# Performance work log

Hardware: AMD Instinct MI355X
Metric: run time of the kernel (lower is better)

## Reference

```python
import jax, jax.numpy as jnp
import numpy as np

DIM = 512
HEADS = 8
DH = DIM // HEADS          # 64, dim_head = dim // 8
M = DIM // 2               # 256 landmarks
ITERS = 6                  # pinv iterations
KS = 33                    # residual depthwise conv kernel (lucidrains default)
N_LAYERS = 2
LN_EPS = 1e-5


def layer_norm(x, scale, bias):
    mu = x.mean(-1, keepdims=True)
    var = ((x - mu) ** 2).mean(-1, keepdims=True)
    return (x - mu) * jax.lax.rsqrt(var + LN_EPS) * scale + bias


def sinusoidal_pe(T, d, dtype):
    pos = np.arange(T)[:, None]
    div = np.exp(np.arange(0, d, 2) * (-np.log(10000.0) / d))
    pe = np.zeros((T, d), dtype=np.float32)
    pe[:, 0::2] = np.sin(pos * div)
    pe[:, 1::2] = np.cos(pos * div)
    return jnp.asarray(pe, dtype=dtype)


def iter_pinv(x):
    # Newton-Schulz Moore-Penrose iteration (lucidrains), global-max scaling
    ax = jnp.abs(x)
    denom = ax.sum(-1).max() * ax.sum(-2).max()
    z = jnp.swapaxes(x, -1, -2) / denom
    I = jnp.eye(x.shape[-1], dtype=x.dtype)
    for _ in range(ITERS):
        xz = x @ z
        z = 0.25 * (z @ (13.0 * I - xz @ (15.0 * I - xz @ (7.0 * I - xz))))
    return z


def nystrom_attention(x, qkv_w, out_w, out_b, conv_w):
    b, n, d = x.shape
    pad = (-n) % M                       # left-pad so seq divisible by M
    xp = jnp.pad(x, ((0, 0), (pad, 0), (0, 0)))
    N = n + pad
    q, k, v = [t.reshape(b, N, HEADS, DH).transpose(0, 2, 1, 3)
               for t in jnp.split(xp @ qkv_w, 3, axis=-1)]  # each [b,h,N,dh]
    q = q * (DH ** -0.5)
    l = N // M                           # segment length per landmark
    q_l = q.reshape(b, HEADS, M, l, DH).mean(3)   # [b,h,M,dh]
    k_l = k.reshape(b, HEADS, M, l, DH).mean(3)
    attn1 = jax.nn.softmax(jnp.einsum('bhid,bhjd->bhij', q, k_l), -1)    # [b,h,N,M]
    attn2 = jax.nn.softmax(jnp.einsum('bhid,bhjd->bhij', q_l, k_l), -1)  # [b,h,M,M]
    attn3 = jax.nn.softmax(jnp.einsum('bhid,bhjd->bhij', q_l, k), -1)    # [b,h,M,N]
    out = attn1 @ (iter_pinv(attn2) @ (attn3 @ v))                       # [b,h,N,dh]
    # residual depthwise conv over sequence, per head (groups=heads)
    P = KS // 2
    out = out + jax.lax.conv_general_dilated(
        v, conv_w, (1, 1), ((P, P), (0, 0)),
        dimension_numbers=('NCHW', 'OIHW', 'NCHW'), feature_group_count=HEADS)
    out = out.transpose(0, 2, 1, 3).reshape(b, N, d)
    out = out @ out_w + out_b
    return out[:, -n:]


def setup_inputs() -> dict:
    key = jax.random.key(0)
    ks = jax.random.split(key, 12)
    B, T, IN_DIM = 4, 4095, 1024
    s = 0.02
    return {
        'data': jax.random.normal(ks[0], (B, T, IN_DIM), jnp.float32),
        'fc1_w': jax.random.normal(ks[1], (IN_DIM, DIM), jnp.float32) * s,
        'fc1_b': jnp.zeros((DIM,), jnp.float32),
        'cls_token': jax.random.normal(ks[2], (1, 1, DIM), jnp.float32),
        'ln_scale': jnp.ones((N_LAYERS, DIM), jnp.float32),
        'ln_bias': jnp.zeros((N_LAYERS, DIM), jnp.float32),
        'qkv_w': jax.random.normal(ks[3], (N_LAYERS, DIM, 3 * DIM), jnp.float32) * s,
        'out_w': jax.random.normal(ks[4], (N_LAYERS, DIM, DIM), jnp.float32) * s,
        'out_b': jnp.zeros((N_LAYERS, DIM), jnp.float32),
        'conv_w': jax.random.normal(ks[5], (N_LAYERS, HEADS, 1, KS, 1), jnp.float32) * s,
        'fnorm_scale': jnp.ones((DIM,), jnp.float32),
        'fnorm_bias': jnp.zeros((DIM,), jnp.float32),
        'fcout_w': jax.random.normal(ks[6], (DIM, 1), jnp.float32) * s,
        'fcout_b': jnp.zeros((1,), jnp.float32),
    }


def reference(data, fc1_w, fc1_b, cls_token, ln_scale, ln_bias, qkv_w, out_w,
              out_b, conv_w, fnorm_scale, fnorm_bias, fcout_w, fcout_b):
    B, T, _ = data.shape
    h = jax.nn.relu(data @ fc1_w + fc1_b)
    h = h + sinusoidal_pe(T, DIM, h.dtype)
    cls = jnp.broadcast_to(cls_token, (B, 1, DIM))
    h = jnp.concatenate([cls, h], axis=1)
    for i in range(N_LAYERS):
        h = h + nystrom_attention(layer_norm(h, ln_scale[i], ln_bias[i]),
                                  qkv_w[i], out_w[i], out_b[i], conv_w[i])
    h = layer_norm(h, fnorm_scale, fnorm_bias)
    logits = (h[:, 0] @ fcout_w + fcout_b)[:, 0]
    y_prob = jax.nn.sigmoid(logits)
    y_hat = (y_prob > 0.5).astype(jnp.int32)
    return logits, y_prob, y_hat
```

## Files before the change

kernel.cpp:

```cpp
#include <hip/hip_runtime.h>
#include <math.h>

typedef long long ll;
typedef __attribute__((ext_vector_type(8))) short short8;
typedef __attribute__((ext_vector_type(4))) float f32x4;

#define NBATCH 4
#define TSEQ   4095
#define NTOK   4096
#define DMODEL 512
#define NHEAD  8
#define DHEAD  64
#define NLAND  256
#define INDIM  1024
#define KCONV  33
#define NBH    32
#define NSPLIT 8

__device__ __forceinline__ float bred(float* red, float v, int tid, int op){
  red[tid] = v; __syncthreads();
  for (int s = 128; s > 0; s >>= 1){
    if (tid < s) red[tid] = op ? fmaxf(red[tid], red[tid+s]) : (red[tid] + red[tid+s]);
    __syncthreads();
  }
  float r = red[0];
  __syncthreads();
  return r;
}

__device__ __forceinline__ short f2bf(float f){
  unsigned u = __float_as_uint(f);
  u += 0x7fff + ((u>>16)&1);
  return (short)(u>>16);
}
__device__ __forceinline__ float bf2f(short s){
  return __uint_as_float(((unsigned)(unsigned short)s) << 16);
}

__device__ __forceinline__ void gload16(const void* g, void* l){
  __builtin_amdgcn_global_load_lds((const __attribute__((address_space(1))) void*)g,
                                   (__attribute__((address_space(3))) void*)l, 16, 0, 0);
}

__global__ __launch_bounds__(256) void pe_table_k(float* __restrict__ pe){
  int idx = blockIdx.x*256 + threadIdx.x;
  if (idx >= TSEQ*DMODEL) return;
  int c = idx & 511; int t = idx >> 9;
  const double NEG = -9.210340371976184 / 512.0;
  double div = exp((double)(c & ~1) * NEG);
  float ang = (float)((double)t * div);
  pe[idx] = (c & 1) ? cosf(ang) : sinf(ang);
}

__global__ __launch_bounds__(256) void pe_cls_add_k(float* __restrict__ hb, const float* __restrict__ cls,
                                                    const float* __restrict__ pe){
  ll idx = (ll)blockIdx.x*256 + threadIdx.x;
  int c = (int)(idx & 511);
  ll rn = idx >> 9;
  int n = (int)(rn & 4095);
  if (n == 0) hb[idx] = cls[c];
  else        hb[idx] += pe[(ll)(n-1)*512 + c];
}

__global__ __launch_bounds__(256) void cvt_bf16_k(const float* __restrict__ in, short* __restrict__ out, int n8){
  int idx = blockIdx.x*256 + threadIdx.x;
  for (int i = idx; i < n8; i += gridDim.x*256){
    const f32x4* p = (const f32x4*)(in + (ll)i*8);
    f32x4 a = p[0], b = p[1];
    short8 v;
    v[0]=f2bf(a[0]); v[1]=f2bf(a[1]); v[2]=f2bf(a[2]); v[3]=f2bf(a[3]);
    v[4]=f2bf(b[0]); v[5]=f2bf(b[1]); v[6]=f2bf(b[2]); v[7]=f2bf(b[3]);
    ((short8*)out)[i] = v;
  }
}

__global__ __launch_bounds__(256) void transpose_bf16_k(const float* __restrict__ in, short* __restrict__ out,
                                                        int K, int N, ll sIn, ll sOut){
  __shared__ float t[64][65];
  int L = blockIdx.z;
  in  += (ll)L*sIn;
  out += (ll)L*sOut;
  int n0 = blockIdx.x*64, k0 = blockIdx.y*64;
  int tid = threadIdx.x;
  for (int e = tid; e < 4096; e += 256){
    int r = e >> 6, c = e & 63;
    t[r][c] = in[(ll)(k0 + r)*N + n0 + c];
  }
  __syncthreads();
  for (int e = tid; e < 4096; e += 256){
    int r = e >> 6, c = e & 63;
    out[(ll)(n0 + r)*K + k0 + c] = f2bf(t[c][r]);
  }
}

__global__ __launch_bounds__(256) void ln_rows_k(const float* __restrict__ in, short* __restrict__ out,
                                                 const float* __restrict__ sc, const float* __restrict__ bi){
  __shared__ float red[256];
  ll row = blockIdx.x;
  const float* xr = in + row*DMODEL;
  short* orow = out + row*DMODEL;
  int tid = threadIdx.x;
  float v0 = xr[tid], v1 = xr[tid+256];
  float mu = bred(red, v0+v1, tid, 0) * (1.f/512.f);
  float d0 = v0-mu, d1 = v1-mu;
  float var = bred(red, d0*d0 + d1*d1, tid, 0) * (1.f/512.f);
  float inv = 1.f / sqrtf(var + 1e-5f);
  orow[tid]     = f2bf(d0*inv*sc[tid]     + bi[tid]);
  orow[tid+256] = f2bf(d1*inv*sc[tid+256] + bi[tid+256]);
}

template<int BM, int BN, int AB, int BMODE, int CB, int SW>
__global__ __launch_bounds__(256)
void mgemm(const void* __restrict__ Av, const void* __restrict__ Bv,
           void* __restrict__ Cv, const void* __restrict__ Ev,
           const float* __restrict__ bias,
           int Mr, int K, int lda, int ldb, int ldc,
           ll sA, ll sB, ll sC,
           float c0, float c1, int flags)
{
  constexpr int MI = BM/32, NJ = BN/32;
  __shared__ __align__(16) short As[BM*64];
  __shared__ __align__(16) short Bs[BN*64];
  int z = blockIdx.z;
  int bx = blockIdx.x, by = blockIdx.y;
  if (SW){
    int nwg = gridDim.x*gridDim.y;
    int lin = by*gridDim.x + bx;
    int q = nwg >> 3, r = nwg & 7;
    int xcd = lin & 7, idx = lin >> 3;
    int wg = (xcd < r) ? (xcd*(q+1) + idx) : (r*(q+1) + (xcd - r)*q + idx);
    bx = wg % gridDim.x; by = wg / gridDim.x;
  }
  int n0 = bx*BN, m0 = by*BM;
  int tid = threadIdx.x;
  int lane = tid & 63, w = tid >> 6;
  int wr = w >> 1, wc = w & 1;
  int l15 = lane & 15, l4 = lane >> 4;
  bool fullM = (m0 + BM <= Mr);

  f32x4 acc[MI][NJ];
  #pragma unroll
  for (int i = 0; i < MI; i++)
    #pragma unroll
    for (int j = 0; j < NJ; j++) acc[i][j] = (f32x4){0.f,0.f,0.f,0.f};

  for (int k0 = 0; k0 < K; k0 += 64){
    if (AB && fullM){
      #pragma unroll
      for (int it = 0; it < BM/32; ++it){
        int base = (w*(BM/32) + it)*64;
        int ls = base + lane;
        int row = ls >> 3, slot = ls & 7;
        const short* gp = (const short*)Av + (ll)z*sA + (ll)(m0 + row)*lda + k0 + ((slot ^ (row&7))<<3);
        gload16(gp, (char*)As + (ll)base*16);
      }
    } else {
      #pragma unroll
      for (int it = 0; it < BM/32; ++it){
        int tau = tid + 256*it;
        int row = tau >> 3, slot = tau & 7;
        int grow = m0 + row;
        short8 v;
        if (AB){
          if (grow < Mr) v = *(const short8*)((const short*)Av + (ll)z*sA + (ll)grow*lda + k0 + slot*8);
          else v = (short8){0,0,0,0,0,0,0,0};
        } else {
          f32x4 p0 = {0.f,0.f,0.f,0.f}, p1 = {0.f,0.f,0.f,0.f};
          if (grow < Mr){
            const float* ap = (const float*)Av + (ll)z*sA + (ll)grow*lda + k0 + slot*8;
            p0 = *(const f32x4*)ap; p1 = *(const f32x4*)(ap+4);
          }
          v[0]=f2bf(p0[0]); v[1]=f2bf(p0[1]); v[2]=f2bf(p0[2]); v[3]=f2bf(p0[3]);
          v[4]=f2bf(p1[0]); v[5]=f2bf(p1[1]); v[6]=f2bf(p1[2]); v[7]=f2bf(p1[3]);
        }
        ((short8*)As)[row*8 + (slot ^ (row&7))] = v;
      }
    }
    if (BMODE == 2){
      #pragma unroll
      for (int it = 0; it < BN/32; ++it){
        int base = (w*(BN/32) + it)*64;
        int ls = base + lane;
        int n = ls >> 3, slot = ls & 7;
        const short* gp = (const short*)Bv + (ll)z*sB + (ll)(n0 + n)*ldb + k0 + ((slot ^ (n&7))<<3);
        gload16(gp, (char*)Bs + (ll)base*16);
      }
    } else {
      #pragma unroll
      for (int it = 0; it < BN/32; ++it){
        int tau = tid + 256*it;
        int n = tau & (BN-1), slot = tau >> (BN==128 ? 7 : 6);
        short8 v;
        if (BMODE == 1){
          const short* bp = (const short*)Bv + (ll)z*sB + (ll)(k0 + slot*8)*ldb + n0 + n;
          #pragma unroll
          for (int i = 0; i < 8; i++) v[i] = bp[(ll)i*ldb];
        } else {
          const float* bp = (const float*)Bv + (ll)z*sB + (ll)(k0 + slot*8)*ldb + n0 + n;
          #pragma unroll
          for (int i = 0; i < 8; i++) v[i] = f2bf(bp[(ll)i*ldb]);
        }
        ((short8*)Bs)[n*8 + (slot ^ (n&7))] = v;
      }
    }
    __syncthreads();
    #pragma unroll
    for (int kc = 0; kc < 2; kc++){
      short8 af[MI], bfr[NJ];
      #pragma unroll
      for (int i = 0; i < MI; i++){
        int row = wr*(BM/2) + i*16 + l15;
        int g = kc*4 + l4;
        af[i] = ((short8*)As)[row*8 + (g ^ (row&7))];
      }
      #pragma unroll
      for (int j = 0; j < NJ; j++){
        int col = wc*(BN/2) + j*16 + l15;
        int g = kc*4 + l4;
        bfr[j] = ((short8*)Bs)[col*8 + (g ^ (col&7))];
      }
      #pragma unroll
      for (int i = 0; i < MI; i++)
        #pragma unroll
        for (int j = 0; j < NJ; j++)
          acc[i][j] = __builtin_amdgcn_mfma_f32_16x16x32_bf16(af[i], bfr[j], acc[i][j], 0, 0, 0);
    }
    __syncthreads();
  }

  #pragma unroll
  for (int i = 0; i < MI; i++){
    int rbase = m0 + wr*(BM/2) + i*16 + l4*4;
    #pragma unroll
    for (int j = 0; j < NJ; j++){
      int col = n0 + wc*(BN/2) + j*16 + l15;
      #pragma unroll
      for (int r = 0; r < 4; r++){
        int m = rbase + r;
        if (m >= Mr) continue;
        float v = acc[i][j][r];
        if (flags & 4){
          float ev = CB ? bf2f(((const short*)Ev + (ll)z*sC)[(ll)m*ldc + col])
                        : ((const float*)Ev + (ll)z*sC)[(ll)m*ldc + col];
          v = c0 * ev + c1 * v;
        }
        if (flags & 1) v += bias[col];
        if (flags & 2) v = fmaxf(v, 0.f);
        int om = (flags & 16) ? (m + m/TSEQ + 1) : m;
        ll ci = (ll)z*sC + (ll)om*ldc + col;
        if (CB){
          short* Cs = (short*)Cv;
          if (flags & 8) v += bf2f(Cs[ci]);
          Cs[ci] = f2bf(v);
        } else {
          float* Cf = (float*)Cv;
          if (flags & 8) v += Cf[ci];
          Cf[ci] = v;
        }
      }
    }
  }
}

__global__ __launch_bounds__(256)
void gemm_nt(const short* __restrict__ A, const short* __restrict__ Bm, float* __restrict__ C,
             int lda, int ldb, int ldc,
             ll sAb, ll sAh, ll sBb, ll sBh, ll sCb, ll sCh,
             float alpha)
{
  __shared__ float As[64][65];
  __shared__ float Bs[64][65];
  int z = blockIdx.z; int b = z >> 3; int h = z & 7;
  A  += (ll)b*sAb + (ll)h*sAh;
  Bm += (ll)b*sBb + (ll)h*sBh;
  C  += (ll)b*sCb + (ll)h*sCh;
  int n0 = blockIdx.x*64, m0 = blockIdx.y*64;
  int tid = threadIdx.x;
  int kk = tid & 63, rr = tid >> 6;
  #pragma unroll
  for (int r = 0; r < 16; r++){
    As[rr + 4*r][kk] = bf2f(A [(ll)(m0 + rr + 4*r)*lda + kk]);
    Bs[rr + 4*r][kk] = bf2f(Bm[(ll)(n0 + rr + 4*r)*ldb + kk]);
  }
  __syncthreads();
  int tx = tid & 15, ty = tid >> 4;
  float acc[4][4] = {};
  for (int k = 0; k < 64; k++){
    float a[4], bv[4];
    #pragma unroll
    for (int i = 0; i < 4; i++) a[i] = As[ty + 16*i][k];
    #pragma unroll
    for (int j = 0; j < 4; j++) bv[j] = Bs[tx + 16*j][k];
    #pragma unroll
    for (int i = 0; i < 4; i++)
      #pragma unroll
      for (int j = 0; j < 4; j++)
        acc[i][j] += a[i]*bv[j];
  }
  #pragma unroll
  for (int i = 0; i < 4; i++)
    #pragma unroll
    for (int j = 0; j < 4; j++)
      C[(ll)(m0 + ty + 16*i)*ldc + n0 + tx + 16*j] = alpha * acc[i][j];
}

__global__ __launch_bounds__(256)
void mflash_k(const short* __restrict__ Q, const short* __restrict__ K,
              const short* __restrict__ V, short* __restrict__ O,
              int ldq, int ldk, int ldv, int ldo, int nkeys, float alpha,
              ll sQb, ll sQh, ll sKb, ll sKh, ll sVb, ll sVh, ll sOb, ll sOh)
{
  __shared__ __align__(16) short Qs[64*64];
  __shared__ __align__(16) short Ks[64*64];
  __shared__ __align__(16) short Vs[64*64];
  __shared__ __align__(16) short Ps[64*64];
  __shared__ float Sl[64][68];
  __shared__ float m_l[64], s_l[64], scl[64];
  int z = blockIdx.z; int b = z >> 3; int h = z & 7;
  Q += (ll)b*sQb + (ll)h*sQh;
  K += (ll)b*sKb + (ll)h*sKh;
  V += (ll)b*sVb + (ll)h*sVh;
  O += (ll)b*sOb + (ll)h*sOh;
  int m0 = blockIdx.x*64;
  int tid = threadIdx.x;
  int lane = tid & 63, w = tid >> 6;
  int l15 = lane & 15, l4 = lane >> 4;
  int wr = w >> 1, wc = w & 1;

  #pragma unroll
  for (int it = 0; it < 2; it++){
    int tau = tid + 256*it;
    int row = tau >> 3, slot = tau & 7;
    short8 v = *(const short8*)(Q + (ll)(m0 + row)*ldq + slot*8);
    ((short8*)Qs)[row*8 + (slot ^ (row&7))] = v;
  }
  if (tid < 64){ m_l[tid] = -1e30f; s_l[tid] = 0.f; }
  f32x4 o[2][2];
  #pragma unroll
  for (int i = 0; i < 2; i++)
    #pragma unroll
    for (int j = 0; j < 2; j++) o[i][j] = (f32x4){0.f,0.f,0.f,0.f};

  for (int n0 = 0; n0 < nkeys; n0 += 64){
    __syncthreads();
    #pragma unroll
    for (int it = 0; it < 2; it++){
      int tau = tid + 256*it;
      int row = tau >> 3, slot = tau & 7;
      short8 v = *(const short8*)(K + (ll)(n0 + row)*ldk + slot*8);
      ((short8*)Ks)[row*8 + (slot ^ (row&7))] = v;
    }
    #pragma unroll
    for (int it = 0; it < 2; it++){
      int key = (tid >> 3) + 32*it;
      int d0 = (tid & 7)*8;
      short8 v = *(const short8*)(V + (ll)(n0 + key)*ldv + d0);
      #pragma unroll
      for (int j = 0; j < 8; j++){
        int d = d0 + j;
        Vs[d*64 + (((key>>3) ^ (d&7))<<3) + (key&7)] = v[j];
      }
    }
    __syncthreads();
    f32x4 s[2][2];
    #pragma unroll
    for (int i = 0; i < 2; i++)
      #pragma unroll
      for (int j = 0; j < 2; j++) s[i][j] = (f32x4){0.f,0.f,0.f,0.f};
    #pragma unroll
    for (int kc = 0; kc < 2; kc++){
      short8 aq[2], bk[2];
      int g = kc*4 + l4;
      #pragma unroll
      for (int i = 0; i < 2; i++){
        int row = wr*32 + i*16 + l15;
        aq[i] = ((short8*)Qs)[row*8 + (g ^ (row&7))];
      }
      #pragma unroll
      for (int j = 0; j < 2; j++){
        int key = wc*32 + j*16 + l15;
        bk[j] = ((short8*)Ks)[key*8 + (g ^ (key&7))];
      }
      #pragma unroll
      for (int i = 0; i < 2; i++)
        #pragma unroll
        for (int j = 0; j < 2; j++)
          s[i][j] = __builtin_amdgcn_mfma_f32_16x16x32_bf16(aq[i], bk[j], s[i][j], 0, 0, 0);
    }
    #pragma unroll
    for (int i = 0; i < 2; i++)
      #pragma unroll
      for (int j = 0; j < 2; j++)
        #pragma unroll
        for (int r = 0; r < 4; r++)
          Sl[wr*32 + i*16 + l4*4 + r][wc*32 + j*16 + l15] = s[i][j][r] * alpha;
    __syncthreads();
    {
      int row = tid >> 2, q = tid & 3, cb = q*16;
      float sv[16];
      float cmax = -1e30f;
      #pragma unroll
      for (int cc = 0; cc < 16; cc++){ sv[cc] = Sl[row][cb+cc]; cmax = fmaxf(cmax, sv[cc]); }
      cmax = fmaxf(cmax, __shfl_xor(cmax, 1));
      cmax = fmaxf(cmax, __shfl_xor(cmax, 2));
      float mprev = m_l[row];
      float newm = fmaxf(mprev, cmax);
      float lsum = 0.f;
      short8 pv0, pv1;
      #pragma unroll
      for (int cc = 0; cc < 8; cc++){ float e = expf(sv[cc]-newm); lsum += e; pv0[cc] = f2bf(e); }
      #pragma unroll
      for (int cc = 0; cc < 8; cc++){ float e = expf(sv[8+cc]-newm); lsum += e; pv1[cc] = f2bf(e); }
      lsum += __shfl_xor(lsum, 1);
      lsum += __shfl_xor(lsum, 2);
      ((short8*)Ps)[row*8 + ((2*q)   ^ (row&7))] = pv0;
      ((short8*)Ps)[row*8 + ((2*q+1) ^ (row&7))] = pv1;
      if (q == 0){
        float scale = expf(mprev - newm);
        m_l[row] = newm;
        s_l[row] = s_l[row]*scale + lsum;
        scl[row] = scale;
      }
    }
    __syncthreads();
    #pragma unroll
    for (int i = 0; i < 2; i++)
      #pragma unroll
      for (int r = 0; r < 4; r++){
        float sc = scl[wr*32 + i*16 + l4*4 + r];
        #pragma unroll
        for (int j = 0; j < 2; j++) o[i][j][r] *= sc;
      }
    #pragma unroll
    for (int kc = 0; kc < 2; kc++){
      short8 ap[2], bv[2];
      int g = kc*4 + l4;
      #pragma unroll
      for (int i = 0; i < 2; i++){
        int row = wr*32 + i*16 + l15;
        ap[i] = ((short8*)Ps)[row*8 + (g ^ (row&7))];
      }
      #pragma unroll
      for (int j = 0; j < 2; j++){
        int d = wc*32 + j*16 + l15;
        bv[j] = ((short8*)Vs)[d*8 + (g ^ (d&7))];
      }
      #pragma unroll
      for (int i = 0; i < 2; i++)
        #pragma unroll
        for (int j = 0; j < 2; j++)
          o[i][j] = __builtin_amdgcn_mfma_f32_16x16x32_bf16(ap[i], bv[j], o[i][j], 0, 0, 0);
    }
  }
  #pragma unroll
  for (int i = 0; i < 2; i++)
    #pragma unroll
    for (int j = 0; j < 2; j++)
      #pragma unroll
      for (int r = 0; r < 4; r++){
        int row = wr*32 + i*16 + l4*4 + r;
        int col = wc*32 + j*16 + l15;
        O[(ll)(m0 + row)*ldo + col] = f2bf(o[i][j][r] / s_l[row]);
      }
}

__global__ __launch_bounds__(256)
void mflash3_part_k(const short* __restrict__ Q, const short* __restrict__ K,
                    const short* __restrict__ V,
                    float* __restrict__ po, float* __restrict__ pm, float* __restrict__ pl,
                    int ldq, int ldk, int ldv,
                    ll sQb, ll sQh, ll sKb, ll sKh, ll sVb, ll sVh)
{
  __shared__ __align__(16) short Qs[64*64];
  __shared__ __align__(16) short Ks[64*64];
  __shared__ __align__(16) short Vs[64*64];
  __shared__ __align__(16) short Ps[64*64];
  __shared__ float Sl[64][68];
  __shared__ float m_l[64], s_l[64], scl[64];
  int z = blockIdx.z; int b = z >> 3; int h = z & 7;
  int split = blockIdx.y;
  Q += (ll)b*sQb + (ll)h*sQh;
  K += (ll)b*sKb + (ll)h*sKh;
  V += (ll)b*sVb + (ll)h*sVh;
  int m0 = blockIdx.x*64;
  int koff = split * (NTOK/NSPLIT);
  int tid = threadIdx.x;
  int lane = tid & 63, w = tid >> 6;
  int l15 = lane & 15, l4 = lane >> 4;
  int wr = w >> 1, wc = w & 1;

  #pragma unroll
  for (int it = 0; it < 2; it++){
    int tau = tid + 256*it;
    int row = tau >> 3, slot = tau & 7;
    short8 v = *(const short8*)(Q + (ll)(m0 + row)*ldq + slot*8);
    ((short8*)Qs)[row*8 + (slot ^ (row&7))] = v;
  }
  if (tid < 64){ m_l[tid] = -1e30f; s_l[tid] = 0.f; }
  f32x4 o[2][2];
  #pragma unroll
  for (int i = 0; i < 2; i++)
    #pragma unroll
    for (int j = 0; j < 2; j++) o[i][j] = (f32x4){0.f,0.f,0.f,0.f};

  for (int n0 = koff; n0 < koff + NTOK/NSPLIT; n0 += 64){
    __syncthreads();
    #pragma unroll
    for (int it = 0; it < 2; it++){
      int tau = tid + 256*it;
      int row = tau >> 3, slot = tau & 7;
      short8 v = *(const short8*)(K + (ll)(n0 + row)*ldk + slot*8);
      ((short8*)Ks)[row*8 + (slot ^ (row&7))] = v;
    }
    #pragma unroll
    for (int it = 0; it < 2; it++){
      int key = (tid >> 3) + 32*it;
      int d0 = (tid & 7)*8;
      short8 v = *(const short8*)(V + (ll)(n0 + key)*ldv + d0);
      #pragma unroll
      for (int j = 0; j < 8; j++){
        int d = d0 + j;
        Vs[d*64 + (((key>>3) ^ (d&7))<<3) + (key&7)] = v[j];
      }
    }
    __syncthreads();
    f32x4 s[2][2];
    #pragma unroll
    for (int i = 0; i < 2; i++)
      #pragma unroll
      for (int j = 0; j < 2; j++) s[i][j] = (f32x4){0.f,0.f,0.f,0.f};
    #pragma unroll
    for (int kc = 0; kc < 2; kc++){
      short8 aq[2], bk[2];
      int g = kc*4 + l4;
      #pragma unroll
      for (int i = 0; i < 2; i++){
        int row = wr*32 + i*16 + l15;
        aq[i] = ((short8*)Qs)[row*8 + (g ^ (row&7))];
      }
      #pragma unroll
      for (int j = 0; j < 2; j++){
        int key = wc*32 + j*16 + l15;
        bk[j] = ((short8*)Ks)[key*8 + (g ^ (key&7))];
      }
      #pragma unroll
      for (int i = 0; i < 2; i++)
        #pragma unroll
        for (int j = 0; j < 2; j++)
          s[i][j] = __builtin_amdgcn_mfma_f32_16x16x32_bf16(aq[i], bk[j], s[i][j], 0, 0, 0);
    }
    #pragma unroll
    for (int i = 0; i < 2; i++)
      #pragma unroll
      for (int j = 0; j < 2; j++)
        #pragma unroll
        for (int r = 0; r < 4; r++)
          Sl[wr*32 + i*16 + l4*4 + r][wc*32 + j*16 + l15] = s[i][j][r];
    __syncthreads();
    {
      int row = tid >> 2, q = tid & 3, cb = q*16;
      float sv[16];
      float cmax = -1e30f;
      #pragma unroll
      for (int cc = 0; cc < 16; cc++){ sv[cc] = Sl[row][cb+cc]; cmax = fmaxf(cmax, sv[cc]); }
      cmax = fmaxf(cmax, __shfl_xor(cmax, 1));
      cmax = fmaxf(cmax, __shfl_xor(cmax, 2));
      float mprev = m_l[row];
      float newm = fmaxf(mprev, cmax);
      float lsum = 0.f;
      short8 pv0, pv1;
      #pragma unroll
      for (int cc = 0; cc < 8; cc++){ float e = expf(sv[cc]-newm); lsum += e; pv0[cc] = f2bf(e); }
      #pragma unroll
      for (int cc = 0; cc < 8; cc++){ float e = expf(sv[8+cc]-newm); lsum += e; pv1[cc] = f2bf(e); }
      lsum += __shfl_xor(lsum, 1);
      lsum += __shfl_xor(lsum, 2);
      ((short8*)Ps)[row*8 + ((2*q)   ^ (row&7))] = pv0;
      ((short8*)Ps)[row*8 + ((2*q+1) ^ (row&7))] = pv1;
      if (q == 0){
        float scale = expf(mprev - newm);
        m_l[row] = newm;
        s_l[row] = s_l[row]*scale + lsum;
        scl[row] = scale;
      }
    }
    __syncthreads();
    #pragma unroll
    for (int i = 0; i < 2; i++)
      #pragma unroll
      for (int r = 0; r < 4; r++){
        float sc = scl[wr*32 + i*16 + l4*4 + r];
        #pragma unroll
        for (int j = 0; j < 2; j++) o[i][j][r] *= sc;
      }
    #pragma unroll
    for (int kc = 0; kc < 2; kc++){
      short8 ap[2], bv[2];
      int g = kc*4 + l4;
      #pragma unroll
      for (int i = 0; i < 2; i++){
        int row = wr*32 + i*16 + l15;
        ap[i] = ((short8*)Ps)[row*8 + (g ^ (row&7))];
      }
      #pragma unroll
      for (int j = 0; j < 2; j++){
        int d = wc*32 + j*16 + l15;
        bv[j] = ((short8*)Vs)[d*8 + (g ^ (d&7))];
      }
      #pragma unroll
      for (int i = 0; i < 2; i++)
        #pragma unroll
        for (int j = 0; j < 2; j++)
          o[i][j] = __builtin_amdgcn_mfma_f32_16x16x32_bf16(ap[i], bv[j], o[i][j], 0, 0, 0);
    }
  }
  int bs = z*NSPLIT + split;
  #pragma unroll
  for (int i = 0; i < 2; i++)
    #pragma unroll
    for (int j = 0; j < 2; j++)
      #pragma unroll
      for (int r = 0; r < 4; r++){
        int row = wr*32 + i*16 + l4*4 + r;
        int col = wc*32 + j*16 + l15;
        po[((ll)bs*NLAND + m0 + row)*64 + col] = o[i][j][r];
      }
  if (tid < 64){
    pm[(ll)bs*NLAND + m0 + tid] = m_l[tid];
    pl[(ll)bs*NLAND + m0 + tid] = s_l[tid];
  }
}

__global__ __launch_bounds__(256)
void flash3_comb_k(const float* __restrict__ po, const float* __restrict__ pm,
                   const float* __restrict__ pl, short* __restrict__ av){
  int bh = blockIdx.y;
  int row = blockIdx.x*4 + (threadIdx.x >> 6);
  int col = threadIdx.x & 63;
  float ms = -1e30f;
  float mv[NSPLIT];
  #pragma unroll
  for (int s = 0; s < NSPLIT; s++){
    mv[s] = pm[((ll)bh*NSPLIT + s)*NLAND + row];
    ms = fmaxf(ms, mv[s]);
  }
  float osum = 0.f, lsum = 0.f;
  #pragma unroll
  for (int s = 0; s < NSPLIT; s++){
    float wgt = expf(mv[s] - ms);
    osum += wgt * po[(((ll)bh*NSPLIT + s)*NLAND + row)*64 + col];
    lsum += wgt * pl[((ll)bh*NSPLIT + s)*NLAND + row];
  }
  av[((ll)bh*NLAND + row)*64 + col] = f2bf(osum / lsum);
}

__global__ __launch_bounds__(256) void softmax_rows_k(float* __restrict__ data, short* __restrict__ out16,
                                                      int cols){
  __shared__ float red[256];
  float* row = data + (ll)blockIdx.x * cols;
  short* row16 = out16 ? out16 + (ll)blockIdx.x * cols : nullptr;
  int tid = threadIdx.x;
  float m = -1e30f;
  for (int c = tid; c < cols; c += 256) m = fmaxf(m, row[c]);
  m = bred(red, m, tid, 1);
  float s = 0.f;
  for (int c = tid; c < cols; c += 256){ float e = expf(row[c] - m); row[c] = e; s += e; }
  s = bred(red, s, tid, 0);
  float inv = 1.f/s;
  for (int c = tid; c < cols; c += 256){
    float p = row[c] * inv;
    row[c] = p;
    if (row16) row16[c] = f2bf(p);
  }
}

__global__ __launch_bounds__(256) void landmarks_k(const short* __restrict__ qkv,
                                                   short* __restrict__ ql, short* __restrict__ kl){
  int idx = blockIdx.x*256 + threadIdx.x;
  int d = idx & 63;
  int i = (idx >> 6) & 255;
  int h = (idx >> 14) & 7;
  int b = idx >> 17;
  const short* base = qkv + ((ll)b*NTOK + (ll)i*16)*1536 + h*64 + d;
  float sq = 0.f, sk = 0.f;
  #pragma unroll
  for (int l = 0; l < 16; l++){ sq += bf2f(base[l*1536]); sk += bf2f(base[l*1536 + 512]); }
  ql[idx] = f2bf(sq * (0.125f/16.f));
  kl[idx] = f2bf(sk * (1.f/16.f));
}

__global__ void init_scal_k(unsigned* s){ s[0] = 0u; s[1] = 0u; }

__global__ __launch_bounds__(256) void a2_maxsums_k(const float* __restrict__ a2, unsigned* __restrict__ gm){
  __shared__ float red[256];
  const float* A = a2 + (ll)blockIdx.x*65536;
  int tid = threadIdx.x;
  float cs = 0.f, rs = 0.f;
  for (int i = 0; i < 256; i++) cs += A[i*256 + tid];
  for (int j = 0; j < 256; j++) rs += A[tid*256 + j];
  float cmax = bred(red, cs, tid, 1);
  float rmax = bred(red, rs, tid, 1);
  if (tid == 0){
    atomicMax(gm + 0, __float_as_uint(rmax));
    atomicMax(gm + 1, __float_as_uint(cmax));
  }
}

__global__ __launch_bounds__(256) void zinit_k(const float* __restrict__ a2, short* __restrict__ z,
                                               const unsigned* __restrict__ gm){
  float inv = 1.f / (__uint_as_float(gm[0]) * __uint_as_float(gm[1]));
  int idx = blockIdx.x*256 + threadIdx.x;
  int j = idx & 255, i = (idx >> 8) & 255, bh = idx >> 16;
  z[idx] = f2bf(a2[(ll)bh*65536 + j*256 + i] * inv);
}

__global__ __launch_bounds__(256) void dwconv_add_k(const short* __restrict__ qkv,
                                                    const float* __restrict__ cw, short* __restrict__ out){
  __shared__ float sv[160][64];
  int z = blockIdx.y; int b = z >> 3; int h = z & 7;
  int t0 = blockIdx.x * 128;
  int tid = threadIdx.x;
  const short* vbase = qkv + (ll)b*NTOK*1536 + 1024 + h*64;
  for (int e8 = tid; e8 < 1280; e8 += 256){
    int r = e8 >> 3, d8 = (e8 & 7)*8;
    int t = t0 - 16 + r;
    short8 v = (t >= 0 && t < NTOK) ? *(const short8*)(vbase + (ll)t*1536 + d8)
                                    : (short8){0,0,0,0,0,0,0,0};
    #pragma unroll
    for (int j = 0; j < 8; j++) sv[r][d8 + j] = bf2f(v[j]);
  }
  float wreg[KCONV];
  #pragma unroll
  for (int kk = 0; kk < KCONV; kk++) wreg[kk] = cw[h*KCONV + kk];
  __syncthreads();
  int d = tid & 63, g = tid >> 6;
  float vals[64];
  #pragma unroll
  for (int j = 0; j < 64; j++) vals[j] = sv[g*32 + j][d];
  short* obase = out + (ll)b*NTOK*512 + h*64 + d;
  #pragma unroll
  for (int t = 0; t < 32; t++){
    float s = 0.f;
    #pragma unroll
    for (int kk = 0; kk < KCONV; kk++) s += vals[t + kk]*wreg[kk];
    ll oi = (ll)(t0 + g*32 + t)*512;
    obase[oi] = f2bf(bf2f(obase[oi]) + s);
  }
}

__global__ __launch_bounds__(256) void head_k(const float* __restrict__ hb, const float* __restrict__ fns,
      const float* __restrict__ fnb, const float* __restrict__ fw, const float* __restrict__ fb,
      float* __restrict__ out){
  __shared__ float red[256];
  int b = blockIdx.x;
  const float* xr = hb + (ll)b*NTOK*DMODEL;
  int tid = threadIdx.x;
  float v0 = xr[tid], v1 = xr[tid+256];
  float mu = bred(red, v0+v1, tid, 0) * (1.f/512.f);
  float d0 = v0-mu, d1 = v1-mu;
  float var = bred(red, d0*d0 + d1*d1, tid, 0) * (1.f/512.f);
  float inv = 1.f/sqrtf(var + 1e-5f);
  float y0 = d0*inv*fns[tid]     + fnb[tid];
  float y1 = d1*inv*fns[tid+256] + fnb[tid+256];
  float dot = bred(red, y0*fw[tid] + y1*fw[tid+256], tid, 0);
  if (tid == 0){
    float logit = dot + fb[0];
    float prob = 1.f/(1.f + expf(-logit));
    out[b] = logit; out[4+b] = prob; out[8+b] = (prob > 0.5f) ? 1.f : 0.f;
  }
}

extern "C" void kernel_launch(void* const* d_in, const int* in_sizes, int n_in,
                              void* d_out, int out_size, void* d_ws, size_t ws_size,
                              hipStream_t stream)
{
  (void)in_sizes; (void)n_in; (void)out_size;
  const float* data  = (const float*)d_in[0];
  const float* fc1_w = (const float*)d_in[1];
  const float* fc1_b = (const float*)d_in[2];
  const float* cls   = (const float*)d_in[3];
  const float* ln_s  = (const float*)d_in[4];
  const float* ln_b  = (const float*)d_in[5];
  const float* qkv_w = (const float*)d_in[6];
  const float* out_w = (const float*)d_in[7];
  const float* out_b = (const float*)d_in[8];
  const float* convw = (const float*)d_in[9];
  const float* fns   = (const float*)d_in[10];
  const float* fnb   = (const float*)d_in[11];
  const float* fcw   = (const float*)d_in[12];
  const float* fcb   = (const float*)d_in[13];
  float* out = (float*)d_out;
  float* ws  = (float*)d_ws;

  float* h    = ws;
  short* xb   = (short*)(h + 8388608);
  short* qkvh = xb + 8388608;
  short* ql   = qkvh + 25165824;
  short* kl   = ql + 524288;
  float* a2f  = (float*)(kl + 524288);
  short* a2h  = (short*)(a2f + 2097152);
  short* zA   = a2h + 2097152;
  short* zB   = zA + 2097152;
  short* t1   = zB + 2097152;
  short* t2   = t1 + 2097152;
  short* t3   = t2 + 2097152;
  short* av   = t3 + 2097152;
  short* y2   = av + 524288;
  float* po   = (float*)(y2 + 524288);
  float* pm   = po + 4194304;
  float* pl   = pm + 65536;
  float* pe   = pl + 65536;
  short* datab = (short*)(pe + 2097152);
  short* fc1t  = datab + 16777216;
  short* qkvt  = fc1t + 524288;
  short* outt  = qkvt + 1572864;
  unsigned* scal = (unsigned*)(outt + 524288);

  const size_t NEED = (size_t)((char*)(scal + 2) - (char*)ws);
  if (ws_size < NEED) return;

  pe_table_k<<<(TSEQ*DMODEL + 255)/256, 256, 0, stream>>>(pe);
  cvt_bf16_k<<<2048, 256, 0, stream>>>(data, datab, (NBATCH*TSEQ*INDIM)/8);
  transpose_bf16_k<<<dim3(8, 16, 1), 256, 0, stream>>>(fc1_w, fc1t, INDIM, DMODEL, 0, 0);
  transpose_bf16_k<<<dim3(24, 8, 2), 256, 0, stream>>>(qkv_w, qkvt, DMODEL, 1536,
                                                       (ll)DMODEL*1536, (ll)1536*DMODEL);
  transpose_bf16_k<<<dim3(8, 8, 2), 256, 0, stream>>>(out_w, outt, DMODEL, DMODEL,
                                                      (ll)DMODEL*DMODEL, (ll)DMODEL*DMODEL);

  mgemm<128,128,1,2,0,1><<<dim3(4, 128, 1), 256, 0, stream>>>(
      datab, fc1t, h, nullptr, fc1_b,
      NBATCH*TSEQ, INDIM, INDIM, INDIM, DMODEL,
      0, 0, 0, 0.f, 0.f, 1|2|16);
  pe_cls_add_k<<<(NBATCH*NTOK*DMODEL)/256, 256, 0, stream>>>(h, cls, pe);

  for (int L = 0; L < 2; L++){
    const float* ob = out_b + (ll)L*DMODEL;
    const float* cw = convw + (ll)L*NHEAD*KCONV;
    const short* qwt = qkvt + (ll)L*1536*DMODEL;
    const short* owt = outt + (ll)L*DMODEL*DMODEL;

    ln_rows_k<<<NBATCH*NTOK, 256, 0, stream>>>(h, xb, ln_s + L*DMODEL, ln_b + L*DMODEL);
    mgemm<128,128,1,2,1,1><<<dim3(12, 128, 1), 256, 0, stream>>>(
        xb, qwt, qkvh, nullptr, nullptr,
        NBATCH*NTOK, DMODEL, DMODEL, DMODEL, 1536,
        0, 0, 0, 0.f, 0.f, 0);
    landmarks_k<<<2048, 256, 0, stream>>>(qkvh, ql, kl);

    gemm_nt<<<dim3(4, 4, NBH), 256, 0, stream>>>(
        ql, kl, a2f, 64, 64, 256,
        131072, 16384, 131072, 16384, 524288, 65536, 1.f);
    softmax_rows_k<<<NBH*NLAND, 256, 0, stream>>>(a2f, a2h, 256);
    init_scal_k<<<1, 1, 0, stream>>>(scal);
    a2_maxsums_k<<<NBH, 256, 0, stream>>>(a2f, scal);
    zinit_k<<<8192, 256, 0, stream>>>(a2f, zA, scal);

    short* zc = zA; short* zn = zB;
    for (int it = 0; it < 6; it++){
      mgemm<64,64,1,1,1,0><<<dim3(4, 4, NBH), 256, 0, stream>>>(
          a2h, zc, t1, nullptr, nullptr, 256, 256, 256, 256, 256,
          65536, 65536, 65536, 0.f, 0.f, 0);
      mgemm<64,64,1,1,1,0><<<dim3(4, 4, NBH), 256, 0, stream>>>(
          t1, t1, t2, t1, nullptr, 256, 256, 256, 256, 256,
          65536, 65536, 65536, 7.f, -1.f, 4);
      mgemm<64,64,1,1,1,0><<<dim3(4, 4, NBH), 256, 0, stream>>>(
          t1, t2, t3, t1, nullptr, 256, 256, 256, 256, 256,
          65536, 65536, 65536, 15.f, -1.f, 4);
      mgemm<64,64,1,1,1,0><<<dim3(4, 4, NBH), 256, 0, stream>>>(
          zc, t3, zn, zc, nullptr, 256, 256, 256, 256, 256,
          65536, 65536, 65536, 3.25f, -0.25f, 4);
      short* tmp = zc; zc = zn; zn = tmp;
    }

    mflash3_part_k<<<dim3(4, NSPLIT, NBH), 256, 0, stream>>>(
        ql, qkvh + 512, qkvh + 1024, po, pm, pl,
        64, 1536, 1536,
        131072, 16384, (ll)NTOK*1536, 64, (ll)NTOK*1536, 64);
    flash3_comb_k<<<dim3(64, NBH), 256, 0, stream>>>(po, pm, pl, av);

    mgemm<64,64,1,1,1,0><<<dim3(1, 4, NBH), 256, 0, stream>>>(
        zc, av, y2, nullptr, nullptr, 256, 256, 256, 64, 64,
        65536, 16384, 16384, 0.f, 0.f, 0);

    mflash_k<<<dim3(64, 1, NBH), 256, 0, stream>>>(
        qkvh, kl, y2, xb,
        1536, 64, 64, 512, NLAND, 0.125f,
        (ll)NTOK*1536, 64, 131072, 16384, 131072, 16384, (ll)NTOK*512, 64);

    dwconv_add_k<<<dim3(32, NBH), 256, 0, stream>>>(qkvh, cw, xb);

    mgemm<128,128,1,2,0,1><<<dim3(4, 128, 1), 256, 0, stream>>>(
        xb, owt, h, nullptr, ob,
        NBATCH*NTOK, DMODEL, DMODEL, DMODEL, DMODEL,
        0, 0, 0, 0.f, 0.f, 1|8);
  }

  head_k<<<4, 256, 0, stream>>>(h, fns, fnb, fcw, fcb, out);
}
```

Before: 1.141 ms.

## Fuse landmark attention, softmax and column-sum, fold PE add into fc1 epilogue

Replaces the scalar gemm_nt, the separate row softmax and the max-sum kernels with one MFMA kernel. That kernel computes the landmark scores, applies the softmax in registers, writes the fp32 and bf16 copies, and emits partial column sums. The pinv scaling now uses only the column-sum max, since softmax row sums are 1. The positional-encoding add moves into the fc1 GEMM epilogue, and a tiny kernel writes the cls rows. The landmark kernel is vectorised, and s_setprio hints are added around the MFMA loops in the flash kernels. The aim is to remove several full passes over the hidden state and the attention matrix, at the cost of a slightly different pinv scaling numerically.

```diff
diff --git a/kernel.cpp b/kernel.cpp
--- a/kernel.cpp
+++ b/kernel.cpp
@@ -52,14 +52,10 @@
   pe[idx] = (c & 1) ? cosf(ang) : sinf(ang);
 }
 
-__global__ __launch_bounds__(256) void pe_cls_add_k(float* __restrict__ hb, const float* __restrict__ cls,
-                                                    const float* __restrict__ pe){
-  ll idx = (ll)blockIdx.x*256 + threadIdx.x;
-  int c = (int)(idx & 511);
-  ll rn = idx >> 9;
-  int n = (int)(rn & 4095);
-  if (n == 0) hb[idx] = cls[c];
-  else        hb[idx] += pe[(ll)(n-1)*512 + c];
+__global__ __launch_bounds__(256) void cls_k(float* __restrict__ h, const float* __restrict__ cls){
+  int b = blockIdx.x; int tid = threadIdx.x;
+  h[(ll)b*NTOK*DMODEL + tid]       = cls[tid];
+  h[(ll)b*NTOK*DMODEL + 256 + tid] = cls[256 + tid];
 }
 
 __global__ __launch_bounds__(256) void cvt_bf16_k(const float* __restrict__ in, short* __restrict__ out, int n8){
@@ -246,7 +242,9 @@
         }
         if (flags & 1) v += bias[col];
         if (flags & 2) v = fmaxf(v, 0.f);
-        int om = (flags & 16) ? (m + m/TSEQ + 1) : m;
+        int bq = m / TSEQ;
+        int om = (flags & 16) ? (m + bq + 1) : m;
+        if (flags & 64) v += ((const float*)Ev)[(ll)(m - bq*TSEQ)*DMODEL + col];
         ll ci = (ll)z*sC + (ll)om*ldc + col;
         if (CB){
           short* Cs = (short*)Cv;
@@ -263,45 +261,186 @@
 }
 
 __global__ __launch_bounds__(256)
-void gemm_nt(const short* __restrict__ A, const short* __restrict__ Bm, float* __restrict__ C,
-             int lda, int ldb, int ldc,
-             ll sAb, ll sAh, ll sBb, ll sBh, ll sCb, ll sCh,
-             float alpha)
+void a2_fused_k(const short* __restrict__ ql, const short* __restrict__ kl,
+                float* __restrict__ a2f, short* __restrict__ a2h,
+                float* __restrict__ cspart)
 {
-  __shared__ float As[64][65];
-  __shared__ float Bs[64][65];
-  int z = blockIdx.z; int b = z >> 3; int h = z & 7;
-  A  += (ll)b*sAb + (ll)h*sAh;
-  Bm += (ll)b*sBb + (ll)h*sBh;
-  C  += (ll)b*sCb + (ll)h*sCh;
-  int n0 = blockIdx.x*64, m0 = blockIdx.y*64;
+  __shared__ __align__(16) short Qs[64*64];
+  __shared__ __align__(16) short Ks[256*64];
+  __shared__ float rmax[64][2];
+  __shared__ float rsum[64][2];
+  int bh = blockIdx.y, mb = blockIdx.x;
+  int m0 = mb*64;
+  const short* qlp = ql + (ll)bh*16384 + (ll)m0*64;
+  const short* klp = kl + (ll)bh*16384;
+  float* a2fp = a2f + (ll)bh*65536;
+  short* a2hp = a2h + (ll)bh*65536;
   int tid = threadIdx.x;
-  int kk = tid & 63, rr = tid >> 6;
-  #pragma unroll
-  for (int r = 0; r < 16; r++){
-    As[rr + 4*r][kk] = bf2f(A [(ll)(m0 + rr + 4*r)*lda + kk]);
-    Bs[rr + 4*r][kk] = bf2f(Bm[(ll)(n0 + rr + 4*r)*ldb + kk]);
+  int lane = tid & 63, w = tid >> 6;
+  int wr = w >> 1, wc = w & 1;
+  int l15 = lane & 15, l4 = lane >> 4;
+
+  #pragma unroll
+  for (int it = 0; it < 2; it++){
+    int tau = tid + 256*it;
+    int row = tau >> 3, slot = tau & 7;
+    ((short8*)Qs)[row*8 + (slot ^ (row&7))] = *(const short8*)(qlp + (ll)row*64 + slot*8);
+  }
+  #pragma unroll
+  for (int it = 0; it < 8; it++){
+    int tau = tid + 256*it;
+    int row = tau >> 3, slot = tau & 7;
+    ((short8*)Ks)[row*8 + (slot ^ (row&7))] = *(const short8*)(klp + (ll)row*64 + slot*8);
   }
   __syncthreads();
-  int tx = tid & 15, ty = tid >> 4;
-  float acc[4][4] = {};
-  for (int k = 0; k < 64; k++){
-    float a[4], bv[4];
-    #pragma unroll
-    for (int i = 0; i < 4; i++) a[i] = As[ty + 16*i][k];
-    #pragma unroll
-    for (int j = 0; j < 4; j++) bv[j] = Bs[tx + 16*j][k];
-    #pragma unroll
-    for (int i = 0; i < 4; i++)
-      #pragma unroll
-      for (int j = 0; j < 4; j++)
-        acc[i][j] += a[i]*bv[j];
-  }
-  #pragma unroll
-  for (int i = 0; i < 4; i++)
-    #pragma unroll
-    for (int j = 0; j < 4; j++)
-      C[(ll)(m0 + ty + 16*i)*ldc + n0 + tx + 16*j] = alpha * acc[i][j];
+
+  f32x4 s[4][2][2];
+  #pragma unroll
+  for (int c = 0; c < 4; c++)
+    #pragma unroll
+    for (int i = 0; i < 2; i++)
+      #pragma unroll
+      for (int j = 0; j < 2; j++) s[c][i][j] = (f32x4){0.f,0.f,0.f,0.f};
+
+  __builtin_amdgcn_s_setprio(1);
+  #pragma unroll
+  for (int kc = 0; kc < 2; kc++){
+    int g = kc*4 + l4;
+    short8 aq[2];
+    #pragma unroll
+    for (int i = 0; i < 2; i++){
+      int row = wr*32 + i*16 + l15;
+      aq[i] = ((short8*)Qs)[row*8 + (g ^ (row&7))];
+    }
+    #pragma unroll
+    for (int c = 0; c < 4; c++){
+      short8 bk[2];
+      #pragma unroll
+      for (int j = 0; j < 2; j++){
+        int key = c*64 + wc*32 + j*16 + l15;
+        bk[j] = ((short8*)Ks)[key*8 + (g ^ (key&7))];
+      }
+      #pragma unroll
+      for (int i = 0; i < 2; i++)
+        #pragma unroll
+        for (int j = 0; j < 2; j++)
+          s[c][i][j] = __builtin_amdgcn_mfma_f32_16x16x32_bf16(aq[i], bk[j], s[c][i][j], 0, 0, 0);
+    }
+  }
+  __builtin_amdgcn_s_setprio(0);
+
+  float mrow[2][4];
+  #pragma unroll
+  for (int i = 0; i < 2; i++)
+    #pragma unroll
+    for (int r = 0; r < 4; r++){
+      float m = -1e30f;
+      #pragma unroll
+      for (int c = 0; c < 4; c++)
+        #pragma unroll
+        for (int j = 0; j < 2; j++) m = fmaxf(m, s[c][i][j][r]);
+      m = fmaxf(m, __shfl_xor(m, 1));
+      m = fmaxf(m, __shfl_xor(m, 2));
+      m = fmaxf(m, __shfl_xor(m, 4));
+      m = fmaxf(m, __shfl_xor(m, 8));
+      mrow[i][r] = m;
+    }
+  if (l15 == 0){
+    #pragma unroll
+    for (int i = 0; i < 2; i++)
+      #pragma unroll
+      for (int r = 0; r < 4; r++)
+        rmax[wr*32 + i*16 + l4*4 + r][wc] = mrow[i][r];
+  }
+  __syncthreads();
+  float lsum[2][4];
+  #pragma unroll
+  for (int i = 0; i < 2; i++)
+    #pragma unroll
+    for (int r = 0; r < 4; r++){
+      int row = wr*32 + i*16 + l4*4 + r;
+      float m = fmaxf(rmax[row][0], rmax[row][1]);
+      float ls = 0.f;
+      #pragma unroll
+      for (int c = 0; c < 4; c++)
+        #pragma unroll
+        for (int j = 0; j < 2; j++){
+          float e = expf(s[c][i][j][r] - m);
+          s[c][i][j][r] = e;
+          ls += e;
+        }
+      ls += __shfl_xor(ls, 1);
+      ls += __shfl_xor(ls, 2);
+      ls += __shfl_xor(ls, 4);
+      ls += __shfl_xor(ls, 8);
+      lsum[i][r] = ls;
+    }
+  if (l15 == 0){
+    #pragma unroll
+    for (int i = 0; i < 2; i++)
+      #pragma unroll
+      for (int r = 0; r < 4; r++)
+        rsum[wr*32 + i*16 + l4*4 + r][wc] = lsum[i][r];
+  }
+  __syncthreads();
+  float csum[4][2];
+  #pragma unroll
+  for (int c = 0; c < 4; c++)
+    #pragma unroll
+    for (int j = 0; j < 2; j++) csum[c][j] = 0.f;
+  #pragma unroll
+  for (int i = 0; i < 2; i++)
+    #pragma unroll
+    for (int r = 0; r < 4; r++){
+      int row = wr*32 + i*16 + l4*4 + r;
+      float inv = 1.f/(rsum[row][0] + rsum[row][1]);
+      #pragma unroll
+      for (int c = 0; c < 4; c++)
+        #pragma unroll
+        for (int j = 0; j < 2; j++){
+          float p = s[c][i][j][r] * inv;
+          int col = c*64 + wc*32 + j*16 + l15;
+          a2fp[(ll)(m0 + row)*256 + col] = p;
+          a2hp[(ll)(m0 + row)*256 + col] = f2bf(p);
+          csum[c][j] += p;
+        }
+    }
+  #pragma unroll
+  for (int c = 0; c < 4; c++)
+    #pragma unroll
+    for (int j = 0; j < 2; j++){
+      float v = csum[c][j];
+      v += __shfl_xor(v, 16);
+      v += __shfl_xor(v, 32);
+      csum[c][j] = v;
+    }
+  if (l4 == 0){
+    float* cp = cspart + (ll)(((bh*4 + mb)*2) + wr)*256;
+    #pragma unroll
+    for (int c = 0; c < 4; c++)
+      #pragma unroll
+      for (int j = 0; j < 2; j++)
+        cp[c*64 + wc*32 + j*16 + l15] = csum[c][j];
+  }
+}
+
+__global__ __launch_bounds__(256) void denom_k(const float* __restrict__ cspart, unsigned* __restrict__ scal){
+  __shared__ float red[256];
+  int bh = blockIdx.x;
+  int tid = threadIdx.x;
+  float s = 0.f;
+  #pragma unroll
+  for (int p = 0; p < 8; p++) s += cspart[(ll)(bh*8 + p)*256 + tid];
+  float mx = bred(red, s, tid, 1);
+  if (tid == 0) atomicMax(scal, __float_as_uint(mx));
+}
+
+__global__ __launch_bounds__(256) void zinit_k(const float* __restrict__ a2, short* __restrict__ z,
+                                               const unsigned* __restrict__ gm){
+  float inv = 1.f / __uint_as_float(gm[0]);
+  int idx = blockIdx.x*256 + threadIdx.x;
+  int j = idx & 255, i = (idx >> 8) & 255, bh = idx >> 16;
+  z[idx] = f2bf(a2[(ll)bh*65536 + j*256 + i] * inv);
 }
 
 __global__ __launch_bounds__(256)
@@ -367,6 +506,7 @@
     for (int i = 0; i < 2; i++)
       #pragma unroll
       for (int j = 0; j < 2; j++) s[i][j] = (f32x4){0.f,0.f,0.f,0.f};
+    __builtin_amdgcn_s_setprio(1);
     #pragma unroll
     for (int kc = 0; kc < 2; kc++){
       short8 aq[2], bk[2];
@@ -387,6 +527,7 @@
         for (int j = 0; j < 2; j++)
           s[i][j] = __builtin_amdgcn_mfma_f32_16x16x32_bf16(aq[i], bk[j], s[i][j], 0, 0, 0);
     }
+    __builtin_amdgcn_s_setprio(0);
     #pragma unroll
     for (int i = 0; i < 2; i++)
       #pragma unroll
@@ -431,6 +572,7 @@
         #pragma unroll
         for (int j = 0; j < 2; j++) o[i][j][r] *= sc;
       }
+    __builtin_amdgcn_s_setprio(1);
     #pragma unroll
     for (int kc = 0; kc < 2; kc++){
       short8 ap[2], bv[2];
@@ -451,6 +593,7 @@
         for (int j = 0; j < 2; j++)
           o[i][j] = __builtin_amdgcn_mfma_f32_16x16x32_bf16(ap[i], bv[j], o[i][j], 0, 0, 0);
     }
+    __builtin_amdgcn_s_setprio(0);
   }
   #pragma unroll
   for (int i = 0; i < 2; i++)
@@ -529,6 +672,7 @@
     for (int i = 0; i < 2; i++)
       #pragma unroll
       for (int j = 0; j < 2; j++) s[i][j] = (f32x4){0.f,0.f,0.f,0.f};
+    __builtin_amdgcn_s_setprio(1);
     #pragma unroll
     for (int kc = 0; kc < 2; kc++){
       short8 aq[2], bk[2];
@@ -549,6 +693,7 @@
         for (int j = 0; j < 2; j++)
           s[i][j] = __builtin_amdgcn_mfma_f32_16x16x32_bf16(aq[i], bk[j], s[i][j], 0, 0, 0);
     }
+    __builtin_amdgcn_s_setprio(0);
     #pragma unroll
     for (int i = 0; i < 2; i++)
       #pragma unroll
@@ -593,6 +738,7 @@
         #pragma unroll
         for (int j = 0; j < 2; j++) o[i][j][r] *= sc;
       }
+    __builtin_amdgcn_s_setprio(1);
     #pragma unroll
     for (int kc = 0; kc < 2; kc++){
       short8 ap[2], bv[2];
@@ -613,6 +759,7 @@
         for (int j = 0; j < 2; j++)
           o[i][j] = __builtin_amdgcn_mfma_f32_16x16x32_bf16(ap[i], bv[j], o[i][j], 0, 0, 0);
     }
+    __builtin_amdgcn_s_setprio(0);
   }
   int bs = z*NSPLIT + split;
   #pragma unroll
@@ -654,64 +801,31 @@
   av[((ll)bh*NLAND + row)*64 + col] = f2bf(osum / lsum);
 }
 
-__global__ __launch_bounds__(256) void softmax_rows_k(float* __restrict__ data, short* __restrict__ out16,
-                                                      int cols){
-  __shared__ float red[256];
-  float* row = data + (ll)blockIdx.x * cols;
-  short* row16 = out16 ? out16 + (ll)blockIdx.x * cols : nullptr;
-  int tid = threadIdx.x;
-  float m = -1e30f;
-  for (int c = tid; c < cols; c += 256) m = fmaxf(m, row[c]);
-  m = bred(red, m, tid, 1);
-  float s = 0.f;
-  for (int c = tid; c < cols; c += 256){ float e = expf(row[c] - m); row[c] = e; s += e; }
-  s = bred(red, s, tid, 0);
-  float inv = 1.f/s;
-  for (int c = tid; c < cols; c += 256){
-    float p = row[c] * inv;
-    row[c] = p;
-    if (row16) row16[c] = f2bf(p);
-  }
-}
-
-__global__ __launch_bounds__(256) void landmarks_k(const short* __restrict__ qkv,
-                                                   short* __restrict__ ql, short* __restrict__ kl){
+__global__ __launch_bounds__(256) void landmarks8_k(const short* __restrict__ qkv,
+                                                    short* __restrict__ ql, short* __restrict__ kl){
   int idx = blockIdx.x*256 + threadIdx.x;
-  int d = idx & 63;
-  int i = (idx >> 6) & 255;
-  int h = (idx >> 14) & 7;
-  int b = idx >> 17;
-  const short* base = qkv + ((ll)b*NTOK + (ll)i*16)*1536 + h*64 + d;
-  float sq = 0.f, sk = 0.f;
-  #pragma unroll
-  for (int l = 0; l < 16; l++){ sq += bf2f(base[l*1536]); sk += bf2f(base[l*1536 + 512]); }
-  ql[idx] = f2bf(sq * (0.125f/16.f));
-  kl[idx] = f2bf(sk * (1.f/16.f));
-}
-
-__global__ void init_scal_k(unsigned* s){ s[0] = 0u; s[1] = 0u; }
-
-__global__ __launch_bounds__(256) void a2_maxsums_k(const float* __restrict__ a2, unsigned* __restrict__ gm){
-  __shared__ float red[256];
-  const float* A = a2 + (ll)blockIdx.x*65536;
-  int tid = threadIdx.x;
-  float cs = 0.f, rs = 0.f;
-  for (int i = 0; i < 256; i++) cs += A[i*256 + tid];
-  for (int j = 0; j < 256; j++) rs += A[tid*256 + j];
-  float cmax = bred(red, cs, tid, 1);
-  float rmax = bred(red, rs, tid, 1);
-  if (tid == 0){
-    atomicMax(gm + 0, __float_as_uint(rmax));
-    atomicMax(gm + 1, __float_as_uint(cmax));
-  }
-}
-
-__global__ __launch_bounds__(256) void zinit_k(const float* __restrict__ a2, short* __restrict__ z,
-                                               const unsigned* __restrict__ gm){
-  float inv = 1.f / (__uint_as_float(gm[0]) * __uint_as_float(gm[1]));
-  int idx = blockIdx.x*256 + threadIdx.x;
-  int j = idx & 255, i = (idx >> 8) & 255, bh = idx >> 16;
-  z[idx] = f2bf(a2[(ll)bh*65536 + j*256 + i] * inv);
+  int d8s = idx & 7;
+  int i = (idx >> 3) & 255;
+  int h = (idx >> 11) & 7;
+  int b = idx >> 14;
+  const short* base = qkv + ((ll)b*NTOK + (ll)i*16)*1536 + h*64 + d8s*8;
+  float sq[8] = {}, sk[8] = {};
+  #pragma unroll
+  for (int l = 0; l < 16; l++){
+    short8 vq = *(const short8*)(base + (ll)l*1536);
+    short8 vk = *(const short8*)(base + (ll)l*1536 + 512);
+    #pragma unroll
+    for (int j = 0; j < 8; j++){ sq[j] += bf2f(vq[j]); sk[j] += bf2f(vk[j]); }
+  }
+  short8 oq, ok;
+  #pragma unroll
+  for (int j = 0; j < 8; j++){
+    oq[j] = f2bf(sq[j] * (0.125f/16.f));
+    ok[j] = f2bf(sk[j] * (1.f/16.f));
+  }
+  ll o8 = (ll)((b*8 + h)*256 + i)*8 + d8s;
+  ((short8*)ql)[o8] = oq;
+  ((short8*)kl)[o8] = ok;
 }
 
 __global__ __launch_bounds__(256) void dwconv_add_k(const short* __restrict__ qkv,
@@ -814,7 +928,8 @@
   short* fc1t  = datab + 16777216;
   short* qkvt  = fc1t + 524288;
   short* outt  = qkvt + 1572864;
-  unsigned* scal = (unsigned*)(outt + 524288);
+  float* cspart = (float*)(outt + 524288);
+  unsigned* scal = (unsigned*)(cspart + 65536);
 
   const size_t NEED = (size_t)((char*)(scal + 2) - (char*)ws);
   if (ws_size < NEED) return;
@@ -828,10 +943,10 @@
                                                       (ll)DMODEL*DMODEL, (ll)DMODEL*DMODEL);
 
   mgemm<128,128,1,2,0,1><<<dim3(4, 128, 1), 256, 0, stream>>>(
-      datab, fc1t, h, nullptr, fc1_b,
+      datab, fc1t, h, pe, fc1_b,
       NBATCH*TSEQ, INDIM, INDIM, INDIM, DMODEL,
-      0, 0, 0, 0.f, 0.f, 1|2|16);
-  pe_cls_add_k<<<(NBATCH*NTOK*DMODEL)/256, 256, 0, stream>>>(h, cls, pe);
+      0, 0, 0, 0.f, 0.f, 1|2|16|64);
+  cls_k<<<4, 256, 0, stream>>>(h, cls);
 
   for (int L = 0; L < 2; L++){
     const float* ob = out_b + (ll)L*DMODEL;
@@ -844,14 +959,11 @@
         xb, qwt, qkvh, nullptr, nullptr,
         NBATCH*NTOK, DMODEL, DMODEL, DMODEL, 1536,
         0, 0, 0, 0.f, 0.f, 0);
-    landmarks_k<<<2048, 256, 0, stream>>>(qkvh, ql, kl);
-
-    gemm_nt<<<dim3(4, 4, NBH), 256, 0, stream>>>(
-        ql, kl, a2f, 64, 64, 256,
-        131072, 16384, 131072, 16384, 524288, 65536, 1.f);
-    softmax_rows_k<<<NBH*NLAND, 256, 0, stream>>>(a2f, a2h, 256);
-    init_scal_k<<<1, 1, 0, stream>>>(scal);
-    a2_maxsums_k<<<NBH, 256, 0, stream>>>(a2f, scal);
+    landmarks8_k<<<256, 256, 0, stream>>>(qkvh, ql, kl);
+
+    hipMemsetAsync(scal, 0, sizeof(unsigned), stream);
+    a2_fused_k<<<dim3(4, 32), 256, 0, stream>>>(ql, kl, a2f, a2h, cspart);
+    denom_k<<<32, 256, 0, stream>>>(cspart, scal);
     zinit_k<<<8192, 256, 0, stream>>>(a2f, zA, scal);
 
     short* zc = zA; short* zn = zB;
```

Result: no change. 1.129 ms (-1.1%).
